# Kernel tuning notes

Measured on AMD Instinct MI355X. Metric: run time of the kernel, lower is better.

## Reference

```python
import jax, jax.numpy as jnp
import numpy as np

N, D_IN, D_LAT, K = 200000, 256, 64, 100
ALPHA = 1000.0


def setup_inputs() -> dict:
    key = jax.random.key(0)
    k1, k2, k3, k4 = jax.random.split(key, 4)
    X = jax.random.normal(k1, (N, D_IN), dtype=jnp.float32)
    encoding = jax.random.normal(k2, (N, D_LAT), dtype=jnp.float32)
    decoding = jax.random.normal(k3, (N, D_IN), dtype=jnp.float32)
    # xavier_uniform bound for [K, D]: sqrt(6/(K+D))
    bound = np.sqrt(6.0 / (K + D_LAT)).astype(np.float32)
    centres = jax.random.uniform(k4, (K, D_LAT), dtype=jnp.float32,
                                 minval=-bound, maxval=bound)
    return {"X": X, "encoding": encoding, "decoding": decoding, "centres": centres}


def _cluster_kl(encoding, centres):
    # squared euclidean distances [N, K]
    d2 = (jnp.sum(encoding * encoding, axis=1, keepdims=True)
          + jnp.sum(centres * centres, axis=1)[None, :]
          - 2.0 * encoding @ centres.T)
    d2 = jnp.maximum(d2, 0.0)
    # Student-t (1 dof) soft assignment (DEC)
    q = 1.0 / (1.0 + d2)
    q = q / jnp.sum(q, axis=1, keepdims=True)          # [N, K]
    # target distribution p = (q^2 / f) normalized, detached
    f = jnp.sum(q, axis=0)                              # [K]
    p = (q * q) / f
    p = p / jnp.sum(p, axis=1, keepdims=True)
    p = jax.lax.stop_gradient(p)
    # F.kl_div(log q, p, reduction='batchmean') = sum p*(log p - log q) / N
    kl = jnp.sum(p * (jnp.log(p) - jnp.log(q))) / q.shape[0]
    return kl


def reference(X, encoding, decoding, centres):
    decoder_loss = jnp.mean((X - decoding) ** 2)
    cluster_loss = _cluster_kl(encoding, centres)
    return decoder_loss + cluster_loss * ALPHA
```

## Files before the change

### kernel.cpp

```cpp
#include <hip/hip_runtime.h>

#define N_ROWS 200000
#define D_IN   256
#define D_LAT  64
#define K_CL   100
#define NT     7
#define TPB    256

#define GRPS   3125
#define NMF    625
#define GPB    5

#define SCHUNKS   6250
#define SC_HALF   3125
#define NSTR      512
#define NSLOT     64

typedef __attribute__((ext_vector_type(8))) short bf16x8;
typedef __attribute__((ext_vector_type(4))) float f32x4;

__device__ __forceinline__ float rcpf(float x) { return __builtin_amdgcn_rcpf(x); }

__device__ __forceinline__ short f2bf(float f) {
    union { float f; unsigned u; } v; v.f = f;
    unsigned r = (v.u + 0x7fffu + ((v.u >> 16) & 1u)) >> 16;
    return (short)r;
}

__device__ __forceinline__ void cvt8r(float4 a, float4 b, bf16x8& o, float& sq) {
    sq = fmaf(a.x, a.x, sq); sq = fmaf(a.y, a.y, sq);
    sq = fmaf(a.z, a.z, sq); sq = fmaf(a.w, a.w, sq);
    sq = fmaf(b.x, b.x, sq); sq = fmaf(b.y, b.y, sq);
    sq = fmaf(b.z, b.z, sq); sq = fmaf(b.w, b.w, sq);
    o[0] = f2bf(a.x); o[1] = f2bf(a.y); o[2] = f2bf(a.z); o[3] = f2bf(a.w);
    o[4] = f2bf(b.x); o[5] = f2bf(b.y); o[6] = f2bf(b.z); o[7] = f2bf(b.w);
}

__device__ __forceinline__ void cvt8(const float* __restrict__ p, bf16x8& o, float& sq) {
    float4 a = *(const float4*)p;
    float4 b = *(const float4*)(p + 4);
    cvt8r(a, b, o, sq);
}

#define LANE_IDS()                                                             \
    const int tid = threadIdx.x;                                               \
    const int l   = tid & 63;                                                  \
    const int w   = tid >> 6;                                                  \
    const int c16 = l & 15;                                                    \
    const int g   = l >> 4;

#define PROLOGUE_B()                                                           \
    bf16x8 bfrag[NT][2];                                                       \
    float  cn2v[NT];                                                           \
    _Pragma("unroll")                                                          \
    for (int t = 0; t < NT; ++t) {                                             \
        int col = t * 16 + c16;                                                \
        bool valid = col < K_CL;                                               \
        float sq = 0.f;                                                        \
        _Pragma("unroll")                                                      \
        for (int kt = 0; kt < 2; ++kt) {                                       \
            bf16x8 bf;                                                         \
            if (valid) {                                                       \
                cvt8(cen + col * D_LAT + kt * 32 + g * 8, bf, sq);             \
            } else {                                                           \
                _Pragma("unroll")                                              \
                for (int i = 0; i < 8; ++i) bf[i] = 0;                         \
            }                                                                  \
            bfrag[t][kt] = bf;                                                 \
        }                                                                      \
        sq += __shfl_xor(sq, 16);                                              \
        sq += __shfl_xor(sq, 32);                                              \
        cn2v[t] = sq;                                                          \
    }                                                                          \
    const bool v6 = (c16 < 4);

#define LOADS4(grp, A)                                                         \
    {                                                                          \
        const int rowbase_ = (grp) * 64 + w * 16;                              \
        const float* arow_ = enc + (size_t)(rowbase_ + c16) * D_LAT + g * 8;   \
        A[0] = *(const float4*)(arow_);                                        \
        A[1] = *(const float4*)(arow_ + 4);                                    \
        A[2] = *(const float4*)(arow_ + 32);                                   \
        A[3] = *(const float4*)(arow_ + 36);                                   \
    }

#define GROUP_COMPUTE_FROM(A)                                                  \
    float en2p = 0.f;                                                          \
    bf16x8 afrag0, afrag1;                                                     \
    cvt8r(A[0], A[1], afrag0, en2p);                                           \
    cvt8r(A[2], A[3], afrag1, en2p);                                           \
    en2p += __shfl_xor(en2p, 16);                                              \
    en2p += __shfl_xor(en2p, 32);                                              \
    f32x4 acc[NT];                                                             \
    _Pragma("unroll")                                                          \
    for (int t = 0; t < NT; ++t) {                                             \
        acc[t][0] = 0.f; acc[t][1] = 0.f; acc[t][2] = 0.f; acc[t][3] = 0.f;    \
    }                                                                          \
    _Pragma("unroll")                                                          \
    for (int t = 0; t < NT; ++t)                                               \
        acc[t] = __builtin_amdgcn_mfma_f32_16x16x32_bf16(afrag0, bfrag[t][0], acc[t], 0, 0, 0); \
    _Pragma("unroll")                                                          \
    for (int t = 0; t < NT; ++t)                                               \
        acc[t] = __builtin_amdgcn_mfma_f32_16x16x32_bf16(afrag1, bfrag[t][1], acc[t], 0, 0, 0); \
    float en2r[4];                                                             \
    _Pragma("unroll")                                                          \
    for (int r = 0; r < 4; ++r) en2r[r] = __shfl(en2p, g * 4 + r);             \
    float qv[NT][4];                                                           \
    float rs[4] = {0.f, 0.f, 0.f, 0.f};                                        \
    _Pragma("unroll")                                                          \
    for (int t = 0; t < NT; ++t) {                                             \
        _Pragma("unroll")                                                      \
        for (int r = 0; r < 4; ++r) {                                          \
            float d2 = en2r[r] + cn2v[t] - 2.f * acc[t][r];                    \
            float q = rcpf(1.f + fmaxf(d2, 0.f));                              \
            if (t == 6 && !v6) q = 0.f;                                        \
            qv[t][r] = q; rs[r] += q;                                          \
        }                                                                      \
    }                                                                          \
    _Pragma("unroll")                                                          \
    for (int r = 0; r < 4; ++r) {                                              \
        rs[r] += __shfl_xor(rs[r], 1); rs[r] += __shfl_xor(rs[r], 2);          \
        rs[r] += __shfl_xor(rs[r], 4); rs[r] += __shfl_xor(rs[r], 8);          \
        rs[r] = rcpf(rs[r]);                                                   \
    }

__device__ __forceinline__ void dec_stream(const f32x4* __restrict__ X,
                                           const f32x4* __restrict__ Dec,
                                           double* __restrict__ slots,
                                           int sid, int cbase) {
    float local = 0.f;
#pragma unroll 1
    for (int c = sid; c < SC_HALF; c += NSTR) {
        const int idx = (cbase + c) * 2048 + (int)threadIdx.x;
        f32x4 a[8], b[8];
#pragma unroll
        for (int u = 0; u < 8; ++u)
            a[u] = X[idx + u * 256];
#pragma unroll
        for (int u = 0; u < 8; ++u)
            b[u] = Dec[idx + u * 256];
        __builtin_amdgcn_sched_barrier(0);
#pragma unroll
        for (int u = 0; u < 8; ++u) {
            f32x4 d = a[u] - b[u];
            local = fmaf(d.x, d.x, local); local = fmaf(d.y, d.y, local);
            local = fmaf(d.z, d.z, local); local = fmaf(d.w, d.w, local);
        }
    }
    __shared__ float red[TPB];
    red[threadIdx.x] = local;
    __syncthreads();
    for (int off = TPB / 2; off > 0; off >>= 1) {
        if (threadIdx.x < off) red[threadIdx.x] += red[threadIdx.x + off];
        __syncthreads();
    }
    if (threadIdx.x == 0) atomicAdd(&slots[sid & (NSLOT - 1)], (double)red[0]);
}

__global__ void __launch_bounds__(TPB) k_d1(const f32x4* __restrict__ X,
                                            const f32x4* __restrict__ Xdec,
                                            const float* __restrict__ enc,
                                            const float* __restrict__ cen,
                                            double* __restrict__ dec_slots,
                                            float* __restrict__ fg) {
    if (blockIdx.x >= NMF) {
        dec_stream(X, Xdec, dec_slots, blockIdx.x - NMF, 0);
        return;
    }
    LANE_IDS();
    const int p1id = blockIdx.x;
    float4 abuf[2][4];
    LOADS4(p1id, abuf[0]);
    PROLOGUE_B();
    float facc[NT];
#pragma unroll
    for (int t = 0; t < NT; ++t) facc[t] = 0.f;
#pragma unroll
    for (int j = 0; j < GPB; ++j) {
        if (j + 1 < GPB) LOADS4(p1id + (j + 1) * NMF, abuf[(j + 1) & 1]);
        GROUP_COMPUTE_FROM(abuf[j & 1]);
#pragma unroll
        for (int t = 0; t < NT; ++t) {
            float a = 0.f;
#pragma unroll
            for (int r = 0; r < 4; ++r) a = fmaf(qv[t][r], rs[r], a);
            facc[t] += a;
        }
    }
    __shared__ float f_s[K_CL];
    for (int i = tid; i < K_CL; i += TPB) f_s[i] = 0.f;
    __syncthreads();
#pragma unroll
    for (int t = 0; t < NT; ++t) {
        float a = facc[t];
        a += __shfl_xor(a, 16);
        a += __shfl_xor(a, 32);
        int col = t * 16 + c16;
        if (g == 0 && col < K_CL) atomicAdd(&f_s[col], a);
    }
    __syncthreads();
    for (int i = tid; i < K_CL; i += TPB) atomicAdd(&fg[i], f_s[i]);
}

__global__ void __launch_bounds__(TPB) k_d2(const f32x4* __restrict__ X,
                                            const f32x4* __restrict__ Xdec,
                                            const float* __restrict__ enc,
                                            const float* __restrict__ cen,
                                            const float* __restrict__ fg,
                                            double* __restrict__ dec_slots,
                                            double* __restrict__ kl_slots) {
    if (blockIdx.x >= NMF) {
        dec_stream(X, Xdec, dec_slots, blockIdx.x - NMF, SC_HALF);
        return;
    }
    LANE_IDS();
    const int p2id = blockIdx.x;
    float4 abuf[2][4];
    LOADS4(p2id, abuf[0]);
    PROLOGUE_B();
    float lfv[NT], rfv[NT];
#pragma unroll
    for (int t = 0; t < NT; ++t) {
        int col = t * 16 + c16;
        if (col < K_CL) {
            float fv = fg[col];
            lfv[t] = __logf(fv);
            rfv[t] = rcpf(fv);
        } else { lfv[t] = 0.f; rfv[t] = 0.f; }
    }
    float kl_local = 0.f;
#pragma unroll
    for (int j = 0; j < GPB; ++j) {
        if (j + 1 < GPB) LOADS4(p2id + (j + 1) * NMF, abuf[(j + 1) & 1]);
        GROUP_COMPUTE_FROM(abuf[j & 1]);
        float tac[4] = {0.f, 0.f, 0.f, 0.f};
        float Ap[4]  = {0.f, 0.f, 0.f, 0.f};
        float Bp[4]  = {0.f, 0.f, 0.f, 0.f};
#pragma unroll
        for (int t = 0; t < NT; ++t) {
#pragma unroll
            for (int r = 0; r < 4; ++r) {
                if (t == 6 && !v6) continue;
                float q = qv[t][r] * rs[r];
                float pu = q * q * rfv[t];
                tac[r] += pu;
                Ap[r] = fmaf(pu, __logf(q), Ap[r]);
                Bp[r] = fmaf(pu, lfv[t], Bp[r]);
            }
        }
#pragma unroll
        for (int r = 0; r < 4; ++r) {
            tac[r] += __shfl_xor(tac[r], 1); tac[r] += __shfl_xor(tac[r], 2);
            tac[r] += __shfl_xor(tac[r], 4); tac[r] += __shfl_xor(tac[r], 8);
            Ap[r]  += __shfl_xor(Ap[r], 1);  Ap[r]  += __shfl_xor(Ap[r], 2);
            Ap[r]  += __shfl_xor(Ap[r], 4);  Ap[r]  += __shfl_xor(Ap[r], 8);
            Bp[r]  += __shfl_xor(Bp[r], 1);  Bp[r]  += __shfl_xor(Bp[r], 2);
            Bp[r]  += __shfl_xor(Bp[r], 4);  Bp[r]  += __shfl_xor(Bp[r], 8);
        }
        if (c16 == 0) {
#pragma unroll
            for (int r = 0; r < 4; ++r)
                kl_local += (Ap[r] - Bp[r]) * rcpf(tac[r]) - __logf(tac[r]);
        }
    }
    __shared__ float red[TPB];
    red[tid] = kl_local;
    __syncthreads();
    for (int off = TPB / 2; off > 0; off >>= 1) {
        if (tid < off) red[tid] += red[tid + off];
        __syncthreads();
    }
    if (tid == 0) atomicAdd(&kl_slots[p2id & (NSLOT - 1)], (double)red[0]);
}

__global__ void k_final(const double* __restrict__ dec_s,
                        const double* __restrict__ kl_s,
                        float* __restrict__ out) {
    int l = threadIdx.x;
    double d = dec_s[l];
    double k = kl_s[l];
#pragma unroll
    for (int off = 32; off > 0; off >>= 1) {
        d += __shfl_xor(d, off);
        k += __shfl_xor(k, off);
    }
    if (l == 0)
        out[0] = (float)(d / ((double)N_ROWS * (double)D_IN) + 1000.0 * (k / (double)N_ROWS));
}

extern "C" void kernel_launch(void* const* d_in, const int* in_sizes, int n_in,
                              void* d_out, int out_size, void* d_ws, size_t ws_size,
                              hipStream_t stream) {
    (void)in_sizes; (void)n_in; (void)out_size; (void)ws_size;
    const float* X   = (const float*)d_in[0];
    const float* enc = (const float*)d_in[1];
    const float* dec = (const float*)d_in[2];
    const float* cen = (const float*)d_in[3];
    float* out = (float*)d_out;

    double* dec_slots = (double*)d_ws;
    double* kl_slots  = (double*)((char*)d_ws + 512);
    float*  fg        = (float*)((char*)d_ws + 1024);

    hipMemsetAsync(d_ws, 0, 1536, stream);
    k_d1<<<NMF + NSTR, TPB, 0, stream>>>(
        (const f32x4*)X, (const f32x4*)dec, enc, cen, dec_slots, fg);
    k_d2<<<NMF + NSTR, TPB, 0, stream>>>(
        (const f32x4*)X, (const f32x4*)dec, enc, cen, fg, dec_slots, kl_slots);
    k_final<<<1, 64, 0, stream>>>(dec_slots, kl_slots, out);
}
```

Before: 135.8 us.

## Merge cluster and decoder-stream work into uniform persistent blocks with alternating phase order

Before, each kernel split its grid into two kinds of block: 625 cluster blocks and 512 decoder-stream blocks. Now every one of 1024 blocks does both jobs. Odd blocks run the streaming MSE phase first and even blocks run it last, so memory-bound and compute-bound work interleave across the GPU. The cluster loop becomes a grid-stride double-buffered loop, launch bounds ask for 4 blocks per SM, and the second kernel's streaming loads are nontemporal. This is meant to balance load and overlap bandwidth with MFMA/ALU work, at the risk of register pressure and poorer tail behaviour.

```diff
diff --git a/kernel.cpp b/kernel.cpp
--- a/kernel.cpp
+++ b/kernel.cpp
@@ -7,14 +7,10 @@
 #define NT     7
 #define TPB    256
 
-#define GRPS   3125
-#define NMF    625
-#define GPB    5
-
-#define SCHUNKS   6250
-#define SC_HALF   3125
-#define NSTR      512
-#define NSLOT     64
+#define GRPS    3125
+#define NBLK    1024
+#define SC_HALF 3125
+#define NSLOT   64
 
 typedef __attribute__((ext_vector_type(8))) short bf16x8;
 typedef __attribute__((ext_vector_type(4))) float f32x4;
@@ -40,6 +36,12 @@
     float4 a = *(const float4*)p;
     float4 b = *(const float4*)(p + 4);
     cvt8r(a, b, o, sq);
+}
+
+template<bool NTL>
+__device__ __forceinline__ f32x4 ldf(const f32x4* __restrict__ p) {
+    if constexpr (NTL) return __builtin_nontemporal_load(p);
+    else return *p;
 }
 
 #define LANE_IDS()                                                             \
@@ -124,21 +126,84 @@
         rs[r] = rcpf(rs[r]);                                                   \
     }
 
-__device__ __forceinline__ void dec_stream(const f32x4* __restrict__ X,
-                                           const f32x4* __restrict__ Dec,
-                                           double* __restrict__ slots,
-                                           int sid, int cbase) {
+#define GROUP_LOOP(PROCESS)                                                    \
+    {                                                                          \
+        int grp_ = (int)blockIdx.x;                                            \
+        float4 A0_[4], A1_[4];                                                 \
+        LOADS4(grp_, A0_);                                                     \
+        while (true) {                                                         \
+            int n1_ = grp_ + NBLK;                                             \
+            if (n1_ < GRPS) LOADS4(n1_, A1_);                                  \
+            { PROCESS(A0_); }                                                  \
+            if (n1_ >= GRPS) break;                                            \
+            int n2_ = n1_ + NBLK;                                              \
+            if (n2_ < GRPS) LOADS4(n2_, A0_);                                  \
+            { PROCESS(A1_); }                                                  \
+            if (n2_ >= GRPS) break;                                            \
+            grp_ = n2_;                                                        \
+        }                                                                      \
+    }
+
+#define PROCESS_P1(A)                                                          \
+    {                                                                          \
+        GROUP_COMPUTE_FROM(A);                                                 \
+        _Pragma("unroll")                                                      \
+        for (int t = 0; t < NT; ++t) {                                         \
+            float aa = 0.f;                                                    \
+            _Pragma("unroll")                                                  \
+            for (int r = 0; r < 4; ++r) aa = fmaf(qv[t][r], rs[r], aa);        \
+            facc[t] += aa;                                                     \
+        }                                                                      \
+    }
+
+#define PROCESS_P2(A)                                                          \
+    {                                                                          \
+        GROUP_COMPUTE_FROM(A);                                                 \
+        float tac[4] = {0.f, 0.f, 0.f, 0.f};                                   \
+        float Ap[4]  = {0.f, 0.f, 0.f, 0.f};                                   \
+        float Bp[4]  = {0.f, 0.f, 0.f, 0.f};                                   \
+        _Pragma("unroll")                                                      \
+        for (int t = 0; t < NT; ++t) {                                         \
+            _Pragma("unroll")                                                  \
+            for (int r = 0; r < 4; ++r) {                                      \
+                if (t == 6 && !v6) continue;             \
+                float q = qv[t][r] * rs[r];                                    \
+                float pu = q * q * rfv[t];                                     \
+                tac[r] += pu;                                                  \
+                Ap[r] = fmaf(pu, __logf(q), Ap[r]);                            \
+                Bp[r] = fmaf(pu, lfv[t], Bp[r]);                               \
+            }                                                                  \
+        }                                                                      \
+        _Pragma("unroll")                                                      \
+        for (int r = 0; r < 4; ++r) {                                          \
+            tac[r] += __shfl_xor(tac[r], 1); tac[r] += __shfl_xor(tac[r], 2);  \
+            tac[r] += __shfl_xor(tac[r], 4); tac[r] += __shfl_xor(tac[r], 8);  \
+            Ap[r]  += __shfl_xor(Ap[r], 1);  Ap[r]  += __shfl_xor(Ap[r], 2);   \
+            Ap[r]  += __shfl_xor(Ap[r], 4);  Ap[r]  += __shfl_xor(Ap[r], 8);   \
+            Bp[r]  += __shfl_xor(Bp[r], 1);  Bp[r]  += __shfl_xor(Bp[r], 2);   \
+            Bp[r]  += __shfl_xor(Bp[r], 4);  Bp[r]  += __shfl_xor(Bp[r], 8);   \
+        }                                                                      \
+        if (c16 == 0) {                                                        \
+            _Pragma("unroll")                                                  \
+            for (int r = 0; r < 4; ++r)                                        \
+                kl_local += (Ap[r] - Bp[r]) * rcpf(tac[r]) - __logf(tac[r]);   \
+        }                                                                      \
+    }
+
+template<bool NTL>
+__device__ __forceinline__ void stream_phase(const f32x4* __restrict__ X,
+                                             const f32x4* __restrict__ Dec,
+                                             double* __restrict__ slots,
+                                             int bid, int cbase) {
     float local = 0.f;
 #pragma unroll 1
-    for (int c = sid; c < SC_HALF; c += NSTR) {
+    for (int c = bid; c < SC_HALF; c += NBLK) {
         const int idx = (cbase + c) * 2048 + (int)threadIdx.x;
         f32x4 a[8], b[8];
 #pragma unroll
-        for (int u = 0; u < 8; ++u)
-            a[u] = X[idx + u * 256];
-#pragma unroll
-        for (int u = 0; u < 8; ++u)
-            b[u] = Dec[idx + u * 256];
+        for (int u = 0; u < 8; ++u) a[u] = ldf<NTL>(X + idx + u * 256);
+#pragma unroll
+        for (int u = 0; u < 8; ++u) b[u] = ldf<NTL>(Dec + idx + u * 256);
         __builtin_amdgcn_sched_barrier(0);
 #pragma unroll
         for (int u = 0; u < 8; ++u) {
@@ -147,130 +212,87 @@
             local = fmaf(d.z, d.z, local); local = fmaf(d.w, d.w, local);
         }
     }
-    __shared__ float red[TPB];
-    red[threadIdx.x] = local;
+    __shared__ float sred[TPB];
+    sred[threadIdx.x] = local;
     __syncthreads();
     for (int off = TPB / 2; off > 0; off >>= 1) {
-        if (threadIdx.x < off) red[threadIdx.x] += red[threadIdx.x + off];
-        __syncthreads();
-    }
-    if (threadIdx.x == 0) atomicAdd(&slots[sid & (NSLOT - 1)], (double)red[0]);
-}
-
-__global__ void __launch_bounds__(TPB) k_d1(const f32x4* __restrict__ X,
-                                            const f32x4* __restrict__ Xdec,
-                                            const float* __restrict__ enc,
-                                            const float* __restrict__ cen,
-                                            double* __restrict__ dec_slots,
-                                            float* __restrict__ fg) {
-    if (blockIdx.x >= NMF) {
-        dec_stream(X, Xdec, dec_slots, blockIdx.x - NMF, 0);
-        return;
-    }
+        if (threadIdx.x < off) sred[threadIdx.x] += sred[threadIdx.x + off];
+        __syncthreads();
+    }
+    if (threadIdx.x == 0) atomicAdd(&slots[bid & (NSLOT - 1)], (double)sred[0]);
+    __syncthreads();
+}
+
+__global__ void __launch_bounds__(TPB, 4) k_d1(const f32x4* __restrict__ X,
+                                               const f32x4* __restrict__ Xdec,
+                                               const float* __restrict__ enc,
+                                               const float* __restrict__ cen,
+                                               double* __restrict__ dec_slots,
+                                               float* __restrict__ fg) {
     LANE_IDS();
-    const int p1id = blockIdx.x;
-    float4 abuf[2][4];
-    LOADS4(p1id, abuf[0]);
-    PROLOGUE_B();
-    float facc[NT];
-#pragma unroll
-    for (int t = 0; t < NT; ++t) facc[t] = 0.f;
-#pragma unroll
-    for (int j = 0; j < GPB; ++j) {
-        if (j + 1 < GPB) LOADS4(p1id + (j + 1) * NMF, abuf[(j + 1) & 1]);
-        GROUP_COMPUTE_FROM(abuf[j & 1]);
+    const int bid = blockIdx.x;
+    const bool streamFirst = (bid & 1);
+    if (streamFirst) stream_phase<false>(X, Xdec, dec_slots, bid, 0);
+    {
+        PROLOGUE_B();
+        float facc[NT];
+#pragma unroll
+        for (int t = 0; t < NT; ++t) facc[t] = 0.f;
+        GROUP_LOOP(PROCESS_P1);
+        __shared__ float f_s[K_CL];
+        for (int i = tid; i < K_CL; i += TPB) f_s[i] = 0.f;
+        __syncthreads();
 #pragma unroll
         for (int t = 0; t < NT; ++t) {
-            float a = 0.f;
-#pragma unroll
-            for (int r = 0; r < 4; ++r) a = fmaf(qv[t][r], rs[r], a);
-            facc[t] += a;
+            float a = facc[t];
+            a += __shfl_xor(a, 16);
+            a += __shfl_xor(a, 32);
+            int col = t * 16 + c16;
+            if (g == 0 && col < K_CL) atomicAdd(&f_s[col], a);
         }
-    }
-    __shared__ float f_s[K_CL];
-    for (int i = tid; i < K_CL; i += TPB) f_s[i] = 0.f;
-    __syncthreads();
-#pragma unroll
-    for (int t = 0; t < NT; ++t) {
-        float a = facc[t];
-        a += __shfl_xor(a, 16);
-        a += __shfl_xor(a, 32);
-        int col = t * 16 + c16;
-        if (g == 0 && col < K_CL) atomicAdd(&f_s[col], a);
-    }
-    __syncthreads();
-    for (int i = tid; i < K_CL; i += TPB) atomicAdd(&fg[i], f_s[i]);
-}
-
-__global__ void __launch_bounds__(TPB) k_d2(const f32x4* __restrict__ X,
-                                            const f32x4* __restrict__ Xdec,
-                                            const float* __restrict__ enc,
-                                            const float* __restrict__ cen,
-                                            const float* __restrict__ fg,
-                                            double* __restrict__ dec_slots,
-                                            double* __restrict__ kl_slots) {
-    if (blockIdx.x >= NMF) {
-        dec_stream(X, Xdec, dec_slots, blockIdx.x - NMF, SC_HALF);
-        return;
-    }
+        __syncthreads();
+        for (int i = tid; i < K_CL; i += TPB) atomicAdd(&fg[i], f_s[i]);
+        __syncthreads();
+    }
+    if (!streamFirst) stream_phase<false>(X, Xdec, dec_slots, bid, 0);
+}
+
+__global__ void __launch_bounds__(TPB, 4) k_d2(const f32x4* __restrict__ X,
+                                               const f32x4* __restrict__ Xdec,
+                                               const float* __restrict__ enc,
+                                               const float* __restrict__ cen,
+                                               const float* __restrict__ fg,
+                                               double* __restrict__ dec_slots,
+                                               double* __restrict__ kl_slots) {
     LANE_IDS();
-    const int p2id = blockIdx.x;
-    float4 abuf[2][4];
-    LOADS4(p2id, abuf[0]);
-    PROLOGUE_B();
-    float lfv[NT], rfv[NT];
-#pragma unroll
-    for (int t = 0; t < NT; ++t) {
-        int col = t * 16 + c16;
-        if (col < K_CL) {
-            float fv = fg[col];
-            lfv[t] = __logf(fv);
-            rfv[t] = rcpf(fv);
-        } else { lfv[t] = 0.f; rfv[t] = 0.f; }
-    }
-    float kl_local = 0.f;
-#pragma unroll
-    for (int j = 0; j < GPB; ++j) {
-        if (j + 1 < GPB) LOADS4(p2id + (j + 1) * NMF, abuf[(j + 1) & 1]);
-        GROUP_COMPUTE_FROM(abuf[j & 1]);
-        float tac[4] = {0.f, 0.f, 0.f, 0.f};
-        float Ap[4]  = {0.f, 0.f, 0.f, 0.f};
-        float Bp[4]  = {0.f, 0.f, 0.f, 0.f};
+    const int bid = blockIdx.x;
+    const bool streamFirst = (bid & 1);
+    if (streamFirst) stream_phase<true>(X, Xdec, dec_slots, bid, SC_HALF);
+    {
+        PROLOGUE_B();
+        float lfv[NT], rfv[NT];
 #pragma unroll
         for (int t = 0; t < NT; ++t) {
-#pragma unroll
-            for (int r = 0; r < 4; ++r) {
-                if (t == 6 && !v6) continue;
-                float q = qv[t][r] * rs[r];
-                float pu = q * q * rfv[t];
-                tac[r] += pu;
-                Ap[r] = fmaf(pu, __logf(q), Ap[r]);
-                Bp[r] = fmaf(pu, lfv[t], Bp[r]);
-            }
+            int col = t * 16 + c16;
+            if (col < K_CL) {
+                float fv = fg[col];
+                lfv[t] = __logf(fv);
+                rfv[t] = rcpf(fv);
+            } else { lfv[t] = 0.f; rfv[t] = 0.f; }
         }
-#pragma unroll
-        for (int r = 0; r < 4; ++r) {
-            tac[r] += __shfl_xor(tac[r], 1); tac[r] += __shfl_xor(tac[r], 2);
-            tac[r] += __shfl_xor(tac[r], 4); tac[r] += __shfl_xor(tac[r], 8);
-            Ap[r]  += __shfl_xor(Ap[r], 1);  Ap[r]  += __shfl_xor(Ap[r], 2);
-            Ap[r]  += __shfl_xor(Ap[r], 4);  Ap[r]  += __shfl_xor(Ap[r], 8);
-            Bp[r]  += __shfl_xor(Bp[r], 1);  Bp[r]  += __shfl_xor(Bp[r], 2);
-            Bp[r]  += __shfl_xor(Bp[r], 4);  Bp[r]  += __shfl_xor(Bp[r], 8);
+        float kl_local = 0.f;
+        GROUP_LOOP(PROCESS_P2);
+        __shared__ float red[TPB];
+        red[tid] = kl_local;
+        __syncthreads();
+        for (int off = TPB / 2; off > 0; off >>= 1) {
+            if (tid < off) red[tid] += red[tid + off];
+            __syncthreads();
         }
-        if (c16 == 0) {
-#pragma unroll
-            for (int r = 0; r < 4; ++r)
-                kl_local += (Ap[r] - Bp[r]) * rcpf(tac[r]) - __logf(tac[r]);
-        }
-    }
-    __shared__ float red[TPB];
-    red[tid] = kl_local;
-    __syncthreads();
-    for (int off = TPB / 2; off > 0; off >>= 1) {
-        if (tid < off) red[tid] += red[tid + off];
-        __syncthreads();
-    }
-    if (tid == 0) atomicAdd(&kl_slots[p2id & (NSLOT - 1)], (double)red[0]);
+        if (tid == 0) atomicAdd(&kl_slots[bid & (NSLOT - 1)], (double)red[0]);
+        __syncthreads();
+    }
+    if (!streamFirst) stream_phase<true>(X, Xdec, dec_slots, bid, SC_HALF);
 }
 
 __global__ void k_final(const double* __restrict__ dec_s,
@@ -303,9 +325,9 @@
     float*  fg        = (float*)((char*)d_ws + 1024);
 
     hipMemsetAsync(d_ws, 0, 1536, stream);
-    k_d1<<<NMF + NSTR, TPB, 0, stream>>>(
+    k_d1<<<NBLK, TPB, 0, stream>>>(
         (const f32x4*)X, (const f32x4*)dec, enc, cen, dec_slots, fg);
-    k_d2<<<NMF + NSTR, TPB, 0, stream>>>(
+    k_d2<<<NBLK, TPB, 0, stream>>>(
         (const f32x4*)X, (const f32x4*)dec, enc, cen, fg, dec_slots, kl_slots);
     k_final<<<1, 64, 0, stream>>>(dec_slots, kl_slots, out);
 }
```

Measured after the change: 176.5 us. +29.9%, slower.

## Give each decoder-loss chunk its own block and reduce with wave shuffles

Applied to the files above, without the earlier changes.

The decoder MSE stream is no longer 512 persistent blocks looping over chunks. Each block now handles exactly one 2048-vector chunk, so each launch gets 3125 extra blocks instead of 512. The shared-memory tree reduction with repeated __syncthreads is replaced by wavefront xor-shuffles, and each wave does its own double atomicAdd into a slot. This is meant to raise memory-level parallelism and cut synchronisation overhead, at the cost of more block launches and four times as many atomics per chunk.

```diff
diff --git a/kernel.cpp b/kernel.cpp
--- a/kernel.cpp
+++ b/kernel.cpp
@@ -11,9 +11,7 @@
 #define NMF    625
 #define GPB    5
 
-#define SCHUNKS   6250
 #define SC_HALF   3125
-#define NSTR      512
 #define NSLOT     64
 
 typedef __attribute__((ext_vector_type(8))) short bf16x8;
@@ -127,34 +125,26 @@
 __device__ __forceinline__ void dec_stream(const f32x4* __restrict__ X,
                                            const f32x4* __restrict__ Dec,
                                            double* __restrict__ slots,
-                                           int sid, int cbase) {
+                                           int cidx) {
+    const int idx = cidx * 2048 + (int)threadIdx.x;
+    f32x4 a[8], b[8];
+#pragma unroll
+    for (int u = 0; u < 8; ++u) a[u] = X[idx + u * 256];
+#pragma unroll
+    for (int u = 0; u < 8; ++u) b[u] = Dec[idx + u * 256];
+    __builtin_amdgcn_sched_barrier(0);
     float local = 0.f;
-#pragma unroll 1
-    for (int c = sid; c < SC_HALF; c += NSTR) {
-        const int idx = (cbase + c) * 2048 + (int)threadIdx.x;
-        f32x4 a[8], b[8];
-#pragma unroll
-        for (int u = 0; u < 8; ++u)
-            a[u] = X[idx + u * 256];
-#pragma unroll
-        for (int u = 0; u < 8; ++u)
-            b[u] = Dec[idx + u * 256];
-        __builtin_amdgcn_sched_barrier(0);
-#pragma unroll
-        for (int u = 0; u < 8; ++u) {
-            f32x4 d = a[u] - b[u];
-            local = fmaf(d.x, d.x, local); local = fmaf(d.y, d.y, local);
-            local = fmaf(d.z, d.z, local); local = fmaf(d.w, d.w, local);
-        }
-    }
-    __shared__ float red[TPB];
-    red[threadIdx.x] = local;
-    __syncthreads();
-    for (int off = TPB / 2; off > 0; off >>= 1) {
-        if (threadIdx.x < off) red[threadIdx.x] += red[threadIdx.x + off];
-        __syncthreads();
-    }
-    if (threadIdx.x == 0) atomicAdd(&slots[sid & (NSLOT - 1)], (double)red[0]);
+#pragma unroll
+    for (int u = 0; u < 8; ++u) {
+        f32x4 d = a[u] - b[u];
+        local = fmaf(d.x, d.x, local); local = fmaf(d.y, d.y, local);
+        local = fmaf(d.z, d.z, local); local = fmaf(d.w, d.w, local);
+    }
+    local += __shfl_xor(local, 1);  local += __shfl_xor(local, 2);
+    local += __shfl_xor(local, 4);  local += __shfl_xor(local, 8);
+    local += __shfl_xor(local, 16); local += __shfl_xor(local, 32);
+    if ((threadIdx.x & 63) == 0)
+        atomicAdd(&slots[(cidx + (threadIdx.x >> 6)) & (NSLOT - 1)], (double)local);
 }
 
 __global__ void __launch_bounds__(TPB) k_d1(const f32x4* __restrict__ X,
@@ -164,7 +154,7 @@
                                             double* __restrict__ dec_slots,
                                             float* __restrict__ fg) {
     if (blockIdx.x >= NMF) {
-        dec_stream(X, Xdec, dec_slots, blockIdx.x - NMF, 0);
+        dec_stream(X, Xdec, dec_slots, (int)blockIdx.x - NMF);
         return;
     }
     LANE_IDS();
@@ -210,7 +200,7 @@
                                             double* __restrict__ dec_slots,
                                             double* __restrict__ kl_slots) {
     if (blockIdx.x >= NMF) {
-        dec_stream(X, Xdec, dec_slots, blockIdx.x - NMF, SC_HALF);
+        dec_stream(X, Xdec, dec_slots, SC_HALF + (int)blockIdx.x - NMF);
         return;
     }
     LANE_IDS();
@@ -303,9 +293,9 @@
     float*  fg        = (float*)((char*)d_ws + 1024);
 
     hipMemsetAsync(d_ws, 0, 1536, stream);
-    k_d1<<<NMF + NSTR, TPB, 0, stream>>>(
+    k_d1<<<NMF + SC_HALF, TPB, 0, stream>>>(
         (const f32x4*)X, (const f32x4*)dec, enc, cen, dec_slots, fg);
-    k_d2<<<NMF + NSTR, TPB, 0, stream>>>(
+    k_d2<<<NMF + SC_HALF, TPB, 0, stream>>>(
         (const f32x4*)X, (const f32x4*)dec, enc, cen, fg, dec_slots, kl_slots);
     k_final<<<1, 64, 0, stream>>>(dec_slots, kl_slots, out);
 }
```

After: 145.6 us. +7.2%, slower.
